# Kernel optimization log

Hardware: AMD Instinct MI355X
Metric: run time of the kernel (lower is better)

## Reference

```python
import jax, jax.numpy as jnp
import numpy as np

ACTION_SCALE = 0.01
LOG_STD_MIN, LOG_STD_MAX = -20.0, 2.0


def setup_inputs() -> dict:
    key = jax.random.key(0)
    k1, k2, k3 = jax.random.split(key, 3)
    B, N, D = 8, 1024, 128
    kv = jax.random.normal(k1, (B, N, 4 * D), dtype=jnp.float32)
    positions = jax.random.normal(k2, (B, N, 3), dtype=jnp.float32)
    eps = jax.random.normal(k3, (B, N, 3), dtype=jnp.float32)  # standard-normal sample for rsample
    return {"kv": kv, "positions": positions, "eps": eps}


def reference(kv, positions, eps):
    # Split Atomwise output into mean/std key-value embeddings: each [B, N, D]
    k_mu, v_mu, k_sigma, v_sigma = jnp.split(kv, 4, axis=-1)

    # Low-rank attention-like pairwise scores: [B, N, N]
    rel_shifts_mean = jnp.einsum("bid,bjd->bij", k_mu, v_mu)
    rel_shifts_log_std = jnp.einsum("bid,bjd->bij", k_sigma, v_sigma)

    # All-pairs unit displacement vectors: [B, N, N, 3]
    P = positions[:, :, None, :] - positions[:, None, :, :]
    norm = jnp.linalg.norm(P, axis=-1) + 1e-8
    P = P / norm[..., None]

    # Weighted sum over the j axis (torch dim=-2): [B, N, 3]
    actions_mean = jnp.einsum("bijc,bij->bic", P, rel_shifts_mean)
    actions_log_std = jnp.clip(
        jnp.einsum("bijc,bij->bic", P, rel_shifts_log_std), LOG_STD_MIN, LOG_STD_MAX
    )
    actions_std = jnp.exp(actions_log_std)

    # TanhNormal rsample (training branch) with externally supplied noise eps
    pre_tanh = actions_mean + actions_std * eps
    actions = jnp.tanh(pre_tanh)

    # Normal log-prob minus tanh log-det-Jacobian
    normal_lp = (
        -0.5 * ((pre_tanh - actions_mean) / actions_std) ** 2
        - actions_log_std
        - 0.5 * jnp.log(2.0 * jnp.pi)
    )
    log_det = (
        2.0 * jnp.log(2.0)
        + jax.nn.log_sigmoid(2.0 * pre_tanh)
        + jax.nn.log_sigmoid(-2.0 * pre_tanh)
    )
    log_prob = jnp.sum(normal_lp - log_det, axis=(1, 2))[:, None]  # [B, 1]

    actions = actions * ACTION_SCALE
    # change-of-variables correction for the action_scale factor
    n_dims = pre_tanh.shape[1] * pre_tanh.shape[2]
    log_prob = log_prob - n_dims * jnp.log(ACTION_SCALE)
    return actions, log_prob
```

## Files before the change

kernel.cpp:

```cpp
#include <hip/hip_runtime.h>
#include <math.h>


#define NTOK 1024
#define LPCONST 14147.0828114f

typedef __bf16 bf16x8 __attribute__((ext_vector_type(8)));
typedef float f32x4 __attribute__((ext_vector_type(4)));
#define MFMA(a, b, c) __builtin_amdgcn_mfma_f32_16x16x32_bf16(a, b, c, 0, 0, 0)

__device__ __forceinline__ unsigned short to_bf16(float x) {
    return (unsigned short)((__float_as_uint(x) + 0x8000u) >> 16);
}

template <int CTRL>
__device__ __forceinline__ float dpp_add(float v) {
    int y = __builtin_amdgcn_update_dpp(0, __float_as_int(v), CTRL, 0xf, 0xf, true);
    return v + __int_as_float(y);
}
__device__ __forceinline__ float red16(float v) {
    v = dpp_add<0xB1>(v);
    v = dpp_add<0x4E>(v);
    v = dpp_add<0x141>(v);
    v = dpp_add<0x140>(v);
    return v;
}

__device__ __forceinline__ float softplusf(float z) {
    return z > 20.f ? z : log1pf(expf(z));
}

__global__ __launch_bounds__(256) void prepass_kernel(
    const float* __restrict__ kv, unsigned short* __restrict__ frag,
    float* __restrict__ out)
{
    const int t = blockIdx.x * 256 + threadIdx.x;
    if (t < 8) out[8 * NTOK * 3 + t] = LPCONST;

    const int lane = t & 63;
    const int kc   = (t >> 6) & 3;
    const int tile = (t >> 8) & 63;
    const int b    = (t >> 14) & 7;
    const int side = t >> 17;

    const int row = tile * 16 + (lane & 15);
    const int kof = kc * 32 + (lane >> 4) * 8;
    const float* gp = kv + ((size_t)b * NTOK + row) * 512 + side * 128 + kof;
    const float4 m0 = *(const float4*)gp;
    const float4 m1 = *(const float4*)(gp + 4);
    const float4 s0 = *(const float4*)(gp + 256);
    const float4 s1 = *(const float4*)(gp + 260);

    unsigned short* cp = frag + (size_t)side * 2097152 +
                         (size_t)(b * 64 + tile) * 4096 + kc * 1024 + lane * 8;
    ushort4 h0, h1;
    h0.x = to_bf16(m0.x); h0.y = to_bf16(m0.y); h0.z = to_bf16(m0.z); h0.w = to_bf16(m0.w);
    h1.x = to_bf16(m1.x); h1.y = to_bf16(m1.y); h1.z = to_bf16(m1.z); h1.w = to_bf16(m1.w);
    *(ushort4*)(cp + 0) = h0; *(ushort4*)(cp + 4) = h1;
    h0.x = to_bf16(s0.x); h0.y = to_bf16(s0.y); h0.z = to_bf16(s0.z); h0.w = to_bf16(s0.w);
    h1.x = to_bf16(s1.x); h1.y = to_bf16(s1.y); h1.z = to_bf16(s1.z); h1.w = to_bf16(s1.w);
    *(ushort4*)(cp + 512) = h0; *(ushort4*)(cp + 516) = h1;
}

__global__ __launch_bounds__(512) void actor_kernel(
    const unsigned short* __restrict__ frag, const float* __restrict__ pos,
    const float* __restrict__ eps, float* __restrict__ out)
{
    const int t = threadIdx.x;
    const int w = t >> 6;
    const int lane = t & 63;
    const int q = lane >> 4;
    const int r16 = lane & 15;
    const int itx = blockIdx.x;
    const int b = blockIdx.y;
    const int i0 = itx * 16;

    const unsigned short* fragK = frag;
    const unsigned short* fragV = frag + 2097152;
    const float* posb = pos + (size_t)b * NTOK * 3;

    __shared__ float spos[NTOK * 3];
    __shared__ float wacc[8 * 16 * 6];
    __shared__ float fin[96];

    #pragma unroll
    for (int u = t; u < 768; u += 512)
        *(float4*)&spos[u * 4] = *(const float4*)&posb[u * 4];

    const unsigned short* kp = fragK + (size_t)(b * 64 + itx) * 4096 + lane * 8;
    bf16x8 Km[4], Ks[4];
    #pragma unroll
    for (int kc = 0; kc < 4; ++kc) {
        Km[kc] = *(const bf16x8*)(kp + kc * 1024);
        Ks[kc] = *(const bf16x8*)(kp + kc * 1024 + 512);
    }

    __syncthreads();

    const int i = i0 + r16;
    const float pix = spos[i * 3 + 0];
    const float piy = spos[i * 3 + 1];
    const float piz = spos[i * 3 + 2];

    float am0 = 0.f, am1 = 0.f, am2 = 0.f;
    float al0 = 0.f, al1 = 0.f, al2 = 0.f;

    const unsigned short* vbase =
        fragV + (size_t)(b * 64 + w * 8) * 4096 + lane * 8;

    #pragma unroll 2
    for (int jt = 0; jt < 8; ++jt) {
        const unsigned short* vp = vbase + jt * 4096;
        f32x4 accm = (f32x4){0.f, 0.f, 0.f, 0.f};
        f32x4 accs = (f32x4){0.f, 0.f, 0.f, 0.f};
        #pragma unroll
        for (int kc = 0; kc < 4; ++kc) {
            const bf16x8 Vm = *(const bf16x8*)(vp + kc * 1024);
            const bf16x8 Vs = *(const bf16x8*)(vp + kc * 1024 + 512);
            accm = MFMA(Vm, Km[kc], accm);
            accs = MFMA(Vs, Ks[kc], accs);
        }
        const int jbase = (w * 8 + jt) * 16 + q * 4;
        #pragma unroll
        for (int reg = 0; reg < 4; ++reg) {
            const float* pj = &spos[(jbase + reg) * 3];
            const float dx = pix - pj[0];
            const float dy = piy - pj[1];
            const float dz = piz - pj[2];
            const float d2 = dx * dx + dy * dy + dz * dz;
            const float inv = d2 > 0.f ? rsqrtf(d2) : 0.f;
            const float wm = accm[reg] * inv;
            const float ws = accs[reg] * inv;
            am0 = fmaf(dx, wm, am0); am1 = fmaf(dy, wm, am1); am2 = fmaf(dz, wm, am2);
            al0 = fmaf(dx, ws, al0); al1 = fmaf(dy, ws, al1); al2 = fmaf(dz, ws, al2);
        }
    }

    am0 += __shfl_xor(am0, 16, 64); am0 += __shfl_xor(am0, 32, 64);
    am1 += __shfl_xor(am1, 16, 64); am1 += __shfl_xor(am1, 32, 64);
    am2 += __shfl_xor(am2, 16, 64); am2 += __shfl_xor(am2, 32, 64);
    al0 += __shfl_xor(al0, 16, 64); al0 += __shfl_xor(al0, 32, 64);
    al1 += __shfl_xor(al1, 16, 64); al1 += __shfl_xor(al1, 32, 64);
    al2 += __shfl_xor(al2, 16, 64); al2 += __shfl_xor(al2, 32, 64);

    if (lane < 16) {
        float* p = wacc + (w * 16 + r16) * 6;
        p[0] = am0; p[1] = am1; p[2] = am2; p[3] = al0; p[4] = al1; p[5] = al2;
    }
    __syncthreads();
    if (t < 96) {
        float v = 0.f;
        #pragma unroll
        for (int ww = 0; ww < 8; ++ww) v += wacc[ww * 96 + t];
        fin[t] = v;
    }
    __syncthreads();

    if (t < 16) {
        const int gi = b * NTOK + i0 + t;
        const float* v = fin + t * 6;
        float lp = 0.f;
        #pragma unroll
        for (int c = 0; c < 3; ++c) {
            const float als = fminf(fmaxf(v[3 + c], -20.f), 2.f);
            const float sd = expf(als);
            const float e = eps[gi * 3 + c];
            const float pre = fmaf(sd, e, v[c]);
            out[gi * 3 + c] = tanhf(pre) * 0.01f;
            const float t2 = 2.f * pre;
            lp += -0.5f * e * e - als - 2.3052328944f + softplusf(t2) + softplusf(-t2);
        }
        lp = red16(lp);
        if (t == 0) atomicAdd(out + 8 * NTOK * 3 + b, lp);
    }
}

extern "C" void kernel_launch(void* const* d_in, const int* in_sizes, int n_in,
                              void* d_out, int out_size, void* d_ws, size_t ws_size,
                              hipStream_t stream) {
    const float* kv = (const float*)d_in[0];
    const float* pos = (const float*)d_in[1];
    const float* eps = (const float*)d_in[2];
    float* out = (float*)d_out;
    unsigned short* frag = (unsigned short*)d_ws;

    prepass_kernel<<<dim3(1024), 256, 0, stream>>>(kv, frag, out);
    actor_kernel<<<dim3(64, 8), 512, 0, stream>>>(frag, pos, eps, out);
}
```

Before: 93.58 us.

## Split the j-dimension across two blocks and combine partials with atomics

The grid doubles from 64x8 to 64x2x8 blocks. Each block now covers half of the j tiles, so each wave runs 4 j-iterations instead of 8. Partial sums go into a zeroed global accumulator with atomicAdd, and a per-tile counter picks the last-arriving block to run the TanhNormal epilogue. The goal is better occupancy across CUs (512 blocks instead of 512 waves-worth of 64 blocks per batch), at the cost of extra atomics, fences, a redundant K-fragment load and position staging per block.

```diff
diff --git a/kernel.cpp b/kernel.cpp
--- a/kernel.cpp
+++ b/kernel.cpp
@@ -32,9 +32,12 @@
 
 __global__ __launch_bounds__(256) void prepass_kernel(
     const float* __restrict__ kv, unsigned short* __restrict__ frag,
+    float* __restrict__ acc, unsigned int* __restrict__ counters,
     float* __restrict__ out)
 {
     const int t = blockIdx.x * 256 + threadIdx.x;
+    if (t < 8 * NTOK * 6) acc[t] = 0.f;
+    if (t < 512) counters[t] = 0u;
     if (t < 8) out[8 * NTOK * 3 + t] = LPCONST;
 
     const int lane = t & 63;
@@ -64,7 +67,8 @@
 
 __global__ __launch_bounds__(512) void actor_kernel(
     const unsigned short* __restrict__ frag, const float* __restrict__ pos,
-    const float* __restrict__ eps, float* __restrict__ out)
+    const float* __restrict__ eps, float* __restrict__ acc,
+    unsigned int* __restrict__ counters, float* __restrict__ out)
 {
     const int t = threadIdx.x;
     const int w = t >> 6;
@@ -72,7 +76,8 @@
     const int q = lane >> 4;
     const int r16 = lane & 15;
     const int itx = blockIdx.x;
-    const int b = blockIdx.y;
+    const int jh  = blockIdx.y;
+    const int b   = blockIdx.z;
     const int i0 = itx * 16;
 
     const unsigned short* fragK = frag;
@@ -81,7 +86,7 @@
 
     __shared__ float spos[NTOK * 3];
     __shared__ float wacc[8 * 16 * 6];
-    __shared__ float fin[96];
+    __shared__ unsigned int is_last;
 
     #pragma unroll
     for (int u = t; u < 768; u += 512)
@@ -105,11 +110,12 @@
     float am0 = 0.f, am1 = 0.f, am2 = 0.f;
     float al0 = 0.f, al1 = 0.f, al2 = 0.f;
 
+    const int jtile0 = jh * 32 + w * 4;
     const unsigned short* vbase =
-        fragV + (size_t)(b * 64 + w * 8) * 4096 + lane * 8;
-
-    #pragma unroll 2
-    for (int jt = 0; jt < 8; ++jt) {
+        fragV + (size_t)(b * 64 + jtile0) * 4096 + lane * 8;
+
+    #pragma unroll
+    for (int jt = 0; jt < 4; ++jt) {
         const unsigned short* vp = vbase + jt * 4096;
         f32x4 accm = (f32x4){0.f, 0.f, 0.f, 0.f};
         f32x4 accs = (f32x4){0.f, 0.f, 0.f, 0.f};
@@ -120,7 +126,7 @@
             accm = MFMA(Vm, Km[kc], accm);
             accs = MFMA(Vs, Ks[kc], accs);
         }
-        const int jbase = (w * 8 + jt) * 16 + q * 4;
+        const int jbase = (jtile0 + jt) * 16 + q * 4;
         #pragma unroll
         for (int reg = 0; reg < 4; ++reg) {
             const float* pj = &spos[(jbase + reg) * 3];
@@ -148,30 +154,42 @@
         p[0] = am0; p[1] = am1; p[2] = am2; p[3] = al0; p[4] = al1; p[5] = al2;
     }
     __syncthreads();
+
+    float* accb = acc + ((size_t)b * NTOK + i0) * 6;
     if (t < 96) {
         float v = 0.f;
         #pragma unroll
         for (int ww = 0; ww < 8; ++ww) v += wacc[ww * 96 + t];
-        fin[t] = v;
-    }
-    __syncthreads();
-
-    if (t < 16) {
-        const int gi = b * NTOK + i0 + t;
-        const float* v = fin + t * 6;
-        float lp = 0.f;
-        #pragma unroll
-        for (int c = 0; c < 3; ++c) {
-            const float als = fminf(fmaxf(v[3 + c], -20.f), 2.f);
-            const float sd = expf(als);
-            const float e = eps[gi * 3 + c];
-            const float pre = fmaf(sd, e, v[c]);
-            out[gi * 3 + c] = tanhf(pre) * 0.01f;
-            const float t2 = 2.f * pre;
-            lp += -0.5f * e * e - als - 2.3052328944f + softplusf(t2) + softplusf(-t2);
+        atomicAdd(accb + t, v);
+        __threadfence();
+    }
+    __syncthreads();
+    if (t == 0)
+        is_last = (atomicAdd(&counters[b * 64 + itx], 1u) == 1u);
+    __syncthreads();
+
+    if (is_last) {
+        __threadfence();
+        if (t < 16) {
+            const int gi = b * NTOK + i0 + t;
+            float* ap = accb + t * 6;
+            float vals[6];
+            #pragma unroll
+            for (int c = 0; c < 6; ++c) vals[c] = atomicAdd(ap + c, 0.f);
+            float lp = 0.f;
+            #pragma unroll
+            for (int c = 0; c < 3; ++c) {
+                const float als = fminf(fmaxf(vals[3 + c], -20.f), 2.f);
+                const float sd = expf(als);
+                const float e = eps[gi * 3 + c];
+                const float pre = fmaf(sd, e, vals[c]);
+                out[gi * 3 + c] = tanhf(pre) * 0.01f;
+                const float t2 = 2.f * pre;
+                lp += -0.5f * e * e - als - 2.3052328944f + softplusf(t2) + softplusf(-t2);
+            }
+            lp = red16(lp);
+            if (t == 0) atomicAdd(out + 8 * NTOK * 3 + b, lp);
         }
-        lp = red16(lp);
-        if (t == 0) atomicAdd(out + 8 * NTOK * 3 + b, lp);
     }
 }
 
@@ -183,7 +201,9 @@
     const float* eps = (const float*)d_in[2];
     float* out = (float*)d_out;
     unsigned short* frag = (unsigned short*)d_ws;
-
-    prepass_kernel<<<dim3(1024), 256, 0, stream>>>(kv, frag, out);
-    actor_kernel<<<dim3(64, 8), 512, 0, stream>>>(frag, pos, eps, out);
-}
+    float* acc = (float*)((char*)d_ws + 8388608);
+    unsigned int* counters = (unsigned int*)((char*)d_ws + 8585216);
+
+    prepass_kernel<<<dim3(1024), 256, 0, stream>>>(kv, frag, acc, counters, out);
+    actor_kernel<<<dim3(64, 2, 8), 512, 0, stream>>>(frag, pos, eps, acc, counters, out);
+}
```

Measured after the change: 215.3 us. 2.3x slower.
